# Performance work log

Hardware: AMD Instinct MI355X
Metric: run time of the kernel (lower is better)

## Reference

```python
import jax, jax.numpy as jnp
import numpy as np

B, D, K, H = 8192, 1024, 8, 2048


def setup_inputs() -> dict:
    key = jax.random.key(0)
    ks = jax.random.split(key, 4)
    x = jax.random.normal(ks[0], (B, D), dtype=jnp.float32)
    centroids = jax.random.normal(ks[1], (K, D), dtype=jnp.float32)
    W1 = jax.random.normal(ks[2], (K, D, H), dtype=jnp.float32) / np.sqrt(D).astype(np.float32)
    b1 = jnp.zeros((K, H), dtype=jnp.float32)
    W2 = jax.random.normal(ks[3], (K, H), dtype=jnp.float32) / np.sqrt(H).astype(np.float32)
    b2 = jnp.zeros((K,), dtype=jnp.float32)
    return {"x": x, "centroids": centroids, "W1": W1, "b1": b1, "W2": W2, "b2": b2}


def reference(x, centroids, W1, b1, W2, b2):
    # --- k-means hard routing: nearest centroid per sample (euclidean max_sim) ---
    # d2[b,k] = ||x_b||^2 - 2 x_b . c_k + ||c_k||^2  (avoid [B,K,D] blowup)
    d2 = (jnp.sum(x * x, axis=-1, keepdims=True)
          - 2.0 * (x @ centroids.T)
          + jnp.sum(centroids * centroids, axis=-1)[None, :])  # [B, K]
    cluster = jnp.argmin(d2, axis=-1)  # [B] int, hard assignment

    # --- per-expert log-likelihood heads (Einet stand-in), computed densely ---
    h = jnp.tanh(jnp.einsum("bd,kdh->kbh", x, W1) + b1[:, None, :])  # [K, B, H]
    lls = jnp.einsum("kbh,kh->kb", h, W2) + b2[:, None]              # [K, B]

    # --- combine: each sample takes the LL from its routed expert, original order ---
    lls_sorted = jnp.take_along_axis(lls.T, cluster[:, None], axis=1)[:, 0]  # [B]
    return lls_sorted
```

## Files before the change

### kernel.cpp

```cpp
#include <hip/hip_runtime.h>
#include <hip/hip_bf16.h>
#include <stdint.h>

#define B_N 8192
#define D_N 1024
#define K_N 8
#define H_N 2048

#define BM 352
#define BN 256
#define BK 64
#define GRID_MT 32
#define ABUF 45056
#define BUFSZ 77824
#define RO_OFF 155648
#define PLL_OFF 157056
#define GEMM_LDS 162688

typedef unsigned int u32;
typedef unsigned short u16;
typedef __attribute__((ext_vector_type(8))) short short8;
typedef __attribute__((ext_vector_type(4))) float float4v;

struct __align__(8) us4 { u16 x, y, z, w; };

__device__ __forceinline__ u16 f2bf(float f) {
    union { float f; u32 u; } v; v.f = f;
    u32 u = v.u;
    u32 r = (u + 0x7fffu + ((u >> 16) & 1u)) >> 16;
    return (u16)r;
}

__device__ __forceinline__ float fast_tanh(float x) {
    float t = __expf(2.0f * x);
    return 1.0f - 2.0f * __builtin_amdgcn_rcpf(t + 1.0f);
}

__device__ __forceinline__ void async_copy16(void* lds, const void* g) {
    __builtin_amdgcn_global_load_lds(
        (const __attribute__((address_space(1))) void*)g,
        (__attribute__((address_space(3))) void*)lds, 16, 0, 0);
}

__global__ void route_kernel(const float* __restrict__ x,
                             const float* __restrict__ cent,
                             u16* __restrict__ xbf,
                             int* __restrict__ cluster,
                             u32* __restrict__ counts) {
    int tid = threadIdx.x;
    if (blockIdx.x == 0 && tid < K_N) counts[tid * 32] = 0;
    int wave = tid >> 6, lane = tid & 63;
    int b = blockIdx.x * 4 + wave;
    const float* xr = x + (size_t)b * D_N;

    float4 xv[4];
#pragma unroll
    for (int i = 0; i < 4; ++i)
        xv[i] = *(const float4*)(xr + i * 256 + lane * 4);

#pragma unroll
    for (int i = 0; i < 4; ++i) {
        us4 o;
        o.x = f2bf(xv[i].x); o.y = f2bf(xv[i].y);
        o.z = f2bf(xv[i].z); o.w = f2bf(xv[i].w);
        *(us4*)(xbf + (size_t)b * D_N + i * 256 + lane * 4) = o;
    }

    double acc[K_N];
#pragma unroll
    for (int k = 0; k < K_N; ++k) {
        const float* cr = cent + k * D_N;
        double s = 0.0;
#pragma unroll
        for (int i = 0; i < 4; ++i) {
            float4 cv = *(const float4*)(cr + i * 256 + lane * 4);
            double d0 = (double)xv[i].x - (double)cv.x; s += d0 * d0;
            double d1 = (double)xv[i].y - (double)cv.y; s += d1 * d1;
            double d2 = (double)xv[i].z - (double)cv.z; s += d2 * d2;
            double d3 = (double)xv[i].w - (double)cv.w; s += d3 * d3;
        }
        acc[k] = s;
    }
#pragma unroll
    for (int k = 0; k < K_N; ++k) {
        double v = acc[k];
        for (int off = 32; off; off >>= 1) v += __shfl_down(v, off);
        acc[k] = v;
    }
    if (lane == 0) {
        int best = 0; double bv = acc[0];
#pragma unroll
        for (int k = 1; k < K_N; ++k)
            if (acc[k] < bv) { bv = acc[k]; best = k; }
        cluster[b] = best;
    }
}

__global__ void scatter_kernel(const int* __restrict__ cluster,
                               u32* __restrict__ counts,
                               u32* __restrict__ idxl) {
    __shared__ u32 wcnt[4][K_N];
    __shared__ u32 gb[K_N];
    int tid = threadIdx.x;
    int b = blockIdx.x * 256 + tid;
    int lane = tid & 63, wid = tid >> 6;
    int cl = cluster[b];
    unsigned long long lower = (1ull << lane) - 1ull;
    u32 rank = 0;
#pragma unroll
    for (int k = 0; k < K_N; ++k) {
        unsigned long long mk = __ballot(cl == k);
        if (k == cl) rank = (u32)__popcll(mk & lower);
        if (lane == 0) wcnt[wid][k] = (u32)__popcll(mk);
    }
    __syncthreads();
    if (tid < K_N) {
        u32 tot = wcnt[0][tid] + wcnt[1][tid] + wcnt[2][tid] + wcnt[3][tid];
        gb[tid] = atomicAdd(&counts[tid * 32], tot);
    }
    __syncthreads();
    u32 woff = 0;
    if (wid > 0) woff += wcnt[0][cl];
    if (wid > 1) woff += wcnt[1][cl];
    if (wid > 2) woff += wcnt[2][cl];
    idxl[(size_t)cl * B_N + gb[cl] + woff + rank] = (u32)b;
}

__global__ void w1t_kernel(const float* __restrict__ w1, u16* __restrict__ w1t) {
    __shared__ float ts[64][65];
    int tid = threadIdx.x;
    int h0 = blockIdx.x * 64, d0 = blockIdx.y * 64, k = blockIdx.z;
    const float* src = w1 + ((size_t)k * D_N + d0) * H_N + h0;
#pragma unroll
    for (int i = 0; i < 4; ++i) {
        int q = i * 256 + tid;
        int r = q >> 4, c4 = (q & 15) * 4;
        float4 v = *(const float4*)(src + (size_t)r * H_N + c4);
        ts[c4 + 0][r] = v.x; ts[c4 + 1][r] = v.y;
        ts[c4 + 2][r] = v.z; ts[c4 + 3][r] = v.w;
    }
    __syncthreads();
    u16* dst = w1t + ((size_t)k * H_N + h0) * D_N + d0;
#pragma unroll
    for (int i = 0; i < 4; ++i) {
        int q = i * 256 + tid;
        int hr = q >> 4, d4 = (q & 15) * 4;
        us4 o;
        o.x = f2bf(ts[hr][d4 + 0]); o.y = f2bf(ts[hr][d4 + 1]);
        o.z = f2bf(ts[hr][d4 + 2]); o.w = f2bf(ts[hr][d4 + 3]);
        *(us4*)(dst + (size_t)hr * D_N + d4) = o;
    }
}

__global__ __launch_bounds__(512, 2) void gemm_kernel(
                            const u16* __restrict__ xbf,
                            const u16* __restrict__ w1t,
                            const float* __restrict__ b1,
                            const float* __restrict__ w2,
                            const u32* __restrict__ idxl,
                            const u32* __restrict__ counts,
                            float* __restrict__ llp) {
    extern __shared__ char lds[];
    int k = -1, mt = 0, ntile = 0;
#pragma unroll
    for (int kk = 0; kk < K_N; ++kk) {
        int c = (int)counts[kk * 32];
        int t = (c + BM - 1) / BM;
        if ((int)blockIdx.x >= ntile && (int)blockIdx.x < ntile + t) { k = kk; mt = (int)blockIdx.x - ntile; }
        ntile += t;
    }
    if (k < 0) return;
    int cnt = (int)counts[k * 32];
    int nc = blockIdx.y;
    int rows = cnt - mt * BM; if (rows > BM) rows = BM;
    int tid = threadIdx.x;
    int lane = tid & 63, w = tid >> 6;
    int wm = w >> 2, wn = w & 3;
    int wmbase = wm * 176;
    int h0 = nc * BN;
    int l15 = lane & 15, l4 = lane >> 4;

    u32* ro = (u32*)(lds + RO_OFF);
    float* pll = (float*)(lds + PLL_OFF);

    if (tid < BM) {
        int m = mt * BM + tid;
        int mm = m < cnt ? m : cnt - 1;
        ro[tid] = idxl[(size_t)k * B_N + mm] * (u32)(D_N * 2);
    }
    __syncthreads();

    u32 srcA[6], srcB[4];
#pragma unroll
    for (int i = 0; i < 5; ++i) {
        int c = i * 512 + tid; int r = c >> 3, j = c & 7;
        srcA[i] = ro[r] + ((u32)(j ^ (r & 7)) << 4);
    }
    {
        int c = (tid & 255); int r = 320 + (c >> 3), j = c & 7;
        srcA[5] = ro[r] + ((u32)(j ^ (r & 7)) << 4);
    }
#pragma unroll
    for (int i = 0; i < 4; ++i) {
        int c = i * 512 + tid; int r = c >> 3, j = c & 7;
        srcB[i] = ((u32)(k * H_N + h0 + r) << 11) + ((u32)(j ^ (r & 7)) << 4);
    }
    const char* xb = (const char*)xbf;
    const char* wb = (const char*)w1t;

    float4v acc[11][4];
#pragma unroll
    for (int mf = 0; mf < 11; ++mf)
#pragma unroll
        for (int nf = 0; nf < 4; ++nf)
            acc[mf][nf] = (float4v){0.f, 0.f, 0.f, 0.f};

#pragma unroll
    for (int i = 0; i < 5; ++i)
        async_copy16(lds + i * 8192 + w * 1024, xb + srcA[i]);
    if (w < 4)
        async_copy16(lds + 5 * 8192 + w * 1024, xb + srcA[5]);
#pragma unroll
    for (int i = 0; i < 4; ++i)
        async_copy16(lds + ABUF + i * 8192 + w * 1024, wb + srcB[i]);
    __syncthreads();

    for (int t = 0; t < 16; ++t) {
        char* Acur = lds + (t & 1) * BUFSZ;
        char* Bcur = Acur + ABUF;
        char* Anxt = lds + ((t + 1) & 1) * BUFSZ;
        char* Bnxt = Anxt + ABUF;
        u32 doff = (u32)((t + 1) << 7);
        bool pre = (t < 15);

        if (pre) {
            async_copy16(Anxt + 0 * 8192 + w * 1024, xb + srcA[0] + doff);
            async_copy16(Anxt + 1 * 8192 + w * 1024, xb + srcA[1] + doff);
            async_copy16(Anxt + 2 * 8192 + w * 1024, xb + srcA[2] + doff);
            async_copy16(Anxt + 3 * 8192 + w * 1024, xb + srcA[3] + doff);
            async_copy16(Anxt + 4 * 8192 + w * 1024, xb + srcA[4] + doff);
            if (w < 4)
                async_copy16(Anxt + 5 * 8192 + w * 1024, xb + srcA[5] + doff);
        }

#pragma unroll
        for (int kk = 0; kk < 2; ++kk) {
            short8 bf[4];
#pragma unroll
            for (int nf = 0; nf < 4; ++nf) {
                int rb = wn * 64 + nf * 16 + l15;
                bf[nf] = *(const short8*)(Bcur + rb * 128 + (((kk * 4 + l4) ^ (rb & 7)) << 4));
            }
            if (kk == 1 && pre) {
                async_copy16(Bnxt + 0 * 8192 + w * 1024, wb + srcB[0] + doff);
                async_copy16(Bnxt + 1 * 8192 + w * 1024, wb + srcB[1] + doff);
                async_copy16(Bnxt + 2 * 8192 + w * 1024, wb + srcB[2] + doff);
                async_copy16(Bnxt + 3 * 8192 + w * 1024, wb + srcB[3] + doff);
            }
            __builtin_amdgcn_s_setprio(1);
#pragma unroll
            for (int mf = 0; mf < 11; ++mf) {
                if ((wmbase + mf * 16) < rows) {
                    int r0 = wmbase + mf * 16 + l15;
                    short8 a = *(const short8*)(Acur + r0 * 128 + (((kk * 4 + l4) ^ (r0 & 7)) << 4));
#pragma unroll
                    for (int nf = 0; nf < 4; ++nf)
                        acc[mf][nf] = __builtin_amdgcn_mfma_f32_16x16x32_bf16(a, bf[nf], acc[mf][nf], 0, 0, 0);
                }
            }
            __builtin_amdgcn_s_setprio(0);
        }
        __syncthreads();
    }

    float w2v[4], b1v[4];
#pragma unroll
    for (int nf = 0; nf < 4; ++nf) {
        int h = h0 + wn * 64 + nf * 16 + l15;
        w2v[nf] = w2[k * H_N + h];
        b1v[nf] = b1[k * H_N + h];
    }
#pragma unroll
    for (int mf = 0; mf < 11; ++mf) {
        float rs[4] = {0.f, 0.f, 0.f, 0.f};
#pragma unroll
        for (int nf = 0; nf < 4; ++nf) {
#pragma unroll
            for (int r = 0; r < 4; ++r)
                rs[r] += fast_tanh(acc[mf][nf][r] + b1v[nf]) * w2v[nf];
        }
#pragma unroll
        for (int r = 0; r < 4; ++r) {
            float v = rs[r];
            v += __shfl_xor(v, 8);
            v += __shfl_xor(v, 4);
            v += __shfl_xor(v, 2);
            v += __shfl_xor(v, 1);
            if (l15 == 0) pll[wn * 352 + wmbase + mf * 16 + l4 * 4 + r] = v;
        }
    }
    __syncthreads();
    if (tid < BM) {
        int m = mt * BM + tid;
        if (m < cnt) {
            u32 b = idxl[(size_t)k * B_N + m];
            llp[(size_t)nc * B_N + b] = pll[tid] + pll[352 + tid] + pll[704 + tid] + pll[1056 + tid];
        }
    }
}

__global__ void combine_kernel(const float* __restrict__ llp,
                               const int* __restrict__ cluster,
                               const float* __restrict__ b2,
                               float* __restrict__ out) {
    int b = blockIdx.x * 256 + threadIdx.x;
    float s = b2[cluster[b]];
#pragma unroll
    for (int nc = 0; nc < 8; ++nc) s += llp[(size_t)nc * B_N + b];
    out[b] = s;
}

extern "C" void kernel_launch(void* const* d_in, const int* in_sizes, int n_in,
                              void* d_out, int out_size, void* d_ws, size_t ws_size,
                              hipStream_t stream) {
    const float* x    = (const float*)d_in[0];
    const float* cent = (const float*)d_in[1];
    const float* W1   = (const float*)d_in[2];
    const float* b1   = (const float*)d_in[3];
    const float* W2   = (const float*)d_in[4];
    const float* b2   = (const float*)d_in[5];
    float* out = (float*)d_out;

    char* ws = (char*)d_ws;
    u16* xbf     = (u16*)(ws + 0);
    u16* w1t     = (u16*)(ws + 16777216);
    u32* counts  = (u32*)(ws + 50331648);
    int* cluster = (int*)(ws + 50332672);
    u32* idxl    = (u32*)(ws + 50365440);
    float* llp   = (float*)(ws + 50627584);

    (void)hipFuncSetAttribute((const void*)gemm_kernel,
                              hipFuncAttributeMaxDynamicSharedMemorySize, GEMM_LDS);

    hipLaunchKernelGGL(route_kernel, dim3(B_N / 4), dim3(256), 0, stream,
                       x, cent, xbf, cluster, counts);
    hipLaunchKernelGGL(scatter_kernel, dim3(32), dim3(256), 0, stream,
                       cluster, counts, idxl);
    hipLaunchKernelGGL(w1t_kernel, dim3(H_N / 64, D_N / 64, K_N), dim3(256), 0, stream,
                       W1, w1t);
    hipLaunchKernelGGL(gemm_kernel, dim3(GRID_MT, 8), dim3(512), GEMM_LDS, stream,
                       xbf, w1t, b1, W2, idxl, counts, llp);
    hipLaunchKernelGGL(combine_kernel, dim3(B_N / 256), dim3(256), 0, stream,
                       llp, cluster, b2, out);
}
```

Measured before the change: 87.34 us.

## Switch GEMM to four-stage BK=32 async pipeline with explicit vmcnt waits

Replaces the double-buffered BK=64 main loop with a four-buffer ring of BK=32 tiles, keeping three tiles of loads in flight. __syncthreads is replaced by manual s_waitcnt vmcnt counts plus raw barriers, so each wait covers only the oldest stage. The LDS layout changes so that each 16-row fragment is contiguous, with a new XOR swizzle and a precomputed per-lane fragment offset. The aim is to hide global-load latency more deeply, at the cost of twice as many barriers and hand-tuned wait counts that break if the number of loads per stage changes.

```diff
diff --git a/kernel.cpp b/kernel.cpp
--- a/kernel.cpp
+++ b/kernel.cpp
@@ -9,10 +9,9 @@
 
 #define BM 352
 #define BN 256
-#define BK 64
 #define GRID_MT 32
-#define ABUF 45056
-#define BUFSZ 77824
+#define ABUF 22528
+#define BUFSZ 38912
 #define RO_OFF 155648
 #define PLL_OFF 157056
 #define GEMM_LDS 162688
@@ -190,24 +189,32 @@
     }
     __syncthreads();
 
-    u32 srcA[6], srcB[4];
-#pragma unroll
-    for (int i = 0; i < 5; ++i) {
-        int c = i * 512 + tid; int r = c >> 3, j = c & 7;
-        srcA[i] = ro[r] + ((u32)(j ^ (r & 7)) << 4);
-    }
-    {
-        int c = (tid & 255); int r = 320 + (c >> 3), j = c & 7;
-        srcA[5] = ro[r] + ((u32)(j ^ (r & 7)) << 4);
-    }
-#pragma unroll
-    for (int i = 0; i < 4; ++i) {
-        int c = i * 512 + tid; int r = c >> 3, j = c & 7;
-        srcB[i] = ((u32)(k * H_N + h0 + r) << 11) + ((u32)(j ^ (r & 7)) << 4);
+    u32 srcA[3], srcB[2];
+#pragma unroll
+    for (int i = 0; i < 2; ++i) {
+        int c = (i * 8 + w) * 64 + lane;
+        int row2 = c >> 3, u = (c & 7) ^ (row2 & 7);
+        srcA[i] = ro[row2 * 2 + (u >> 2)] + (u32)((u & 3) << 4);
+    }
+    if (w < 6) {
+        int c = (16 + w) * 64 + lane;
+        int row2 = c >> 3, u = (c & 7) ^ (row2 & 7);
+        srcA[2] = ro[row2 * 2 + (u >> 2)] + (u32)((u & 3) << 4);
+    } else {
+        srcA[2] = 0;
+    }
+#pragma unroll
+    for (int i = 0; i < 2; ++i) {
+        int c = (i * 8 + w) * 64 + lane;
+        int row2 = c >> 3, u = (c & 7) ^ (row2 & 7);
+        srcB[i] = ((u32)(k * H_N + h0 + row2 * 2 + (u >> 2)) << 11) + (u32)((u & 3) << 4);
     }
     const char* xb = (const char*)xbf;
     const char* wb = (const char*)w1t;
 
+    int sw = (((l15 & 1) << 2) | l4) ^ ((l15 >> 1) & 7);
+    u32 foff = (u32)(((l15 >> 1) << 7) | (sw << 4));
+
     float4v acc[11][4];
 #pragma unroll
     for (int mf = 0; mf < 11; ++mf)
@@ -215,63 +222,65 @@
         for (int nf = 0; nf < 4; ++nf)
             acc[mf][nf] = (float4v){0.f, 0.f, 0.f, 0.f};
 
-#pragma unroll
-    for (int i = 0; i < 5; ++i)
-        async_copy16(lds + i * 8192 + w * 1024, xb + srcA[i]);
-    if (w < 4)
-        async_copy16(lds + 5 * 8192 + w * 1024, xb + srcA[5]);
-#pragma unroll
-    for (int i = 0; i < 4; ++i)
-        async_copy16(lds + ABUF + i * 8192 + w * 1024, wb + srcB[i]);
-    __syncthreads();
-
-    for (int t = 0; t < 16; ++t) {
-        char* Acur = lds + (t & 1) * BUFSZ;
-        char* Bcur = Acur + ABUF;
-        char* Anxt = lds + ((t + 1) & 1) * BUFSZ;
-        char* Bnxt = Anxt + ABUF;
-        u32 doff = (u32)((t + 1) << 7);
-        bool pre = (t < 15);
-
-        if (pre) {
-            async_copy16(Anxt + 0 * 8192 + w * 1024, xb + srcA[0] + doff);
-            async_copy16(Anxt + 1 * 8192 + w * 1024, xb + srcA[1] + doff);
-            async_copy16(Anxt + 2 * 8192 + w * 1024, xb + srcA[2] + doff);
-            async_copy16(Anxt + 3 * 8192 + w * 1024, xb + srcA[3] + doff);
-            async_copy16(Anxt + 4 * 8192 + w * 1024, xb + srcA[4] + doff);
-            if (w < 4)
-                async_copy16(Anxt + 5 * 8192 + w * 1024, xb + srcA[5] + doff);
-        }
-
-#pragma unroll
-        for (int kk = 0; kk < 2; ++kk) {
-            short8 bf[4];
-#pragma unroll
-            for (int nf = 0; nf < 4; ++nf) {
-                int rb = wn * 64 + nf * 16 + l15;
-                bf[nf] = *(const short8*)(Bcur + rb * 128 + (((kk * 4 + l4) ^ (rb & 7)) << 4));
+    auto stage_tile = [&](int tt) {
+        char* An = lds + (tt & 3) * BUFSZ;
+        char* Bn = An + ABUF;
+        u32 d = (u32)(tt << 6);
+        async_copy16(An + w * 1024,           xb + srcA[0] + d);
+        async_copy16(An + 8192 + w * 1024,    xb + srcA[1] + d);
+        if (w < 6)
+            async_copy16(An + 16384 + w * 1024, xb + srcA[2] + d);
+        async_copy16(Bn + w * 1024,           wb + srcB[0] + d);
+        async_copy16(Bn + 8192 + w * 1024,    wb + srcB[1] + d);
+    };
+
+    auto compute_tile = [&](int t) {
+        const char* Acur = lds + (t & 3) * BUFSZ;
+        const char* Af = Acur + wmbase * 64 + foff;
+        const char* Bf = Acur + ABUF + (wn << 12) + foff;
+        short8 bfv[4];
+#pragma unroll
+        for (int nf = 0; nf < 4; ++nf)
+            bfv[nf] = *(const short8*)(Bf + nf * 1024);
+        __builtin_amdgcn_s_setprio(1);
+#pragma unroll
+        for (int mf = 0; mf < 11; ++mf) {
+            if ((wmbase + mf * 16) < rows) {
+                short8 a = *(const short8*)(Af + mf * 1024);
+#pragma unroll
+                for (int nf = 0; nf < 4; ++nf)
+                    acc[mf][nf] = __builtin_amdgcn_mfma_f32_16x16x32_bf16(a, bfv[nf], acc[mf][nf], 0, 0, 0);
             }
-            if (kk == 1 && pre) {
-                async_copy16(Bnxt + 0 * 8192 + w * 1024, wb + srcB[0] + doff);
-                async_copy16(Bnxt + 1 * 8192 + w * 1024, wb + srcB[1] + doff);
-                async_copy16(Bnxt + 2 * 8192 + w * 1024, wb + srcB[2] + doff);
-                async_copy16(Bnxt + 3 * 8192 + w * 1024, wb + srcB[3] + doff);
-            }
-            __builtin_amdgcn_s_setprio(1);
-#pragma unroll
-            for (int mf = 0; mf < 11; ++mf) {
-                if ((wmbase + mf * 16) < rows) {
-                    int r0 = wmbase + mf * 16 + l15;
-                    short8 a = *(const short8*)(Acur + r0 * 128 + (((kk * 4 + l4) ^ (r0 & 7)) << 4));
-#pragma unroll
-                    for (int nf = 0; nf < 4; ++nf)
-                        acc[mf][nf] = __builtin_amdgcn_mfma_f32_16x16x32_bf16(a, bf[nf], acc[mf][nf], 0, 0, 0);
-                }
-            }
-            __builtin_amdgcn_s_setprio(0);
-        }
-        __syncthreads();
-    }
+        }
+        __builtin_amdgcn_s_setprio(0);
+    };
+
+#define WAITV(NL, NH) do { \
+        if (w < 6) asm volatile("s_waitcnt vmcnt(" #NL ") lgkmcnt(0)" ::: "memory"); \
+        else       asm volatile("s_waitcnt vmcnt(" #NH ") lgkmcnt(0)" ::: "memory"); \
+    } while (0)
+#define BAR() do { __builtin_amdgcn_s_barrier(); asm volatile("" ::: "memory"); } while (0)
+
+    stage_tile(0); stage_tile(1); stage_tile(2);
+    WAITV(10, 8);
+    BAR();
+
+    for (int t = 0; t < 29; ++t) {
+        stage_tile(t + 3);
+        compute_tile(t);
+        WAITV(10, 8);
+        BAR();
+    }
+    compute_tile(29);
+    WAITV(5, 4);
+    BAR();
+    compute_tile(30);
+    asm volatile("s_waitcnt vmcnt(0) lgkmcnt(0)" ::: "memory");
+    BAR();
+    compute_tile(31);
+
+#undef WAITV
+#undef BAR
 
     float w2v[4], b1v[4];
 #pragma unroll
```

New measurement: 91.94 us. 1.05x slower.

## Restructure GEMM main loop into four barrier-pinned phases with interleaved async loads

Applied to the files above, without the earlier changes.

Shrinks the M tile from 352 to 320 rows (10 MFMA fragments per wave instead of 11) and rewrites the K loop into four explicit phases. Each phase loads its A/B fragments from LDS, issues a slice of the next tile's global-to-LDS async copies, waits on lgkmcnt, then runs 20 MFMAs at raised priority. The aim is a fixed LDS-read/MFMA/copy interleave that spreads global traffic across the iteration, at the cost of more raw barriers and more M tiles in the grid.

```diff
diff --git a/kernel.cpp b/kernel.cpp
--- a/kernel.cpp
+++ b/kernel.cpp
@@ -7,15 +7,15 @@
 #define K_N 8
 #define H_N 2048
 
-#define BM 352
+#define BM 320
 #define BN 256
 #define BK 64
-#define GRID_MT 32
-#define ABUF 45056
-#define BUFSZ 77824
-#define RO_OFF 155648
-#define PLL_OFF 157056
-#define GEMM_LDS 162688
+#define GRID_MT 34
+#define ABYTES 40960
+#define BUFSZ 73728
+#define RO_OFF 147456
+#define PLL_OFF 148736
+#define GEMM_LDS 153856
 
 typedef unsigned int u32;
 typedef unsigned short u16;
@@ -176,7 +176,7 @@
     int tid = threadIdx.x;
     int lane = tid & 63, w = tid >> 6;
     int wm = w >> 2, wn = w & 3;
-    int wmbase = wm * 176;
+    int wmbase = wm * 160;
     int h0 = nc * BN;
     int l15 = lane & 15, l4 = lane >> 4;
 
@@ -190,16 +190,12 @@
     }
     __syncthreads();
 
-    u32 srcA[6], srcB[4];
+    u32 srcA[5], srcB[4];
 #pragma unroll
     for (int i = 0; i < 5; ++i) {
         int c = i * 512 + tid; int r = c >> 3, j = c & 7;
         srcA[i] = ro[r] + ((u32)(j ^ (r & 7)) << 4);
     }
-    {
-        int c = (tid & 255); int r = 320 + (c >> 3), j = c & 7;
-        srcA[5] = ro[r] + ((u32)(j ^ (r & 7)) << 4);
-    }
 #pragma unroll
     for (int i = 0; i < 4; ++i) {
         int c = i * 512 + tid; int r = c >> 3, j = c & 7;
@@ -208,70 +204,101 @@
     const char* xb = (const char*)xbf;
     const char* wb = (const char*)w1t;
 
-    float4v acc[11][4];
-#pragma unroll
-    for (int mf = 0; mf < 11; ++mf)
+    int swz = l15 & 7;
+    u32 aB0 = (u32)((wmbase + l15) * 128 + (((0 + l4) ^ swz) << 4));
+    u32 aB1 = (u32)((wmbase + l15) * 128 + (((4 + l4) ^ swz) << 4));
+    u32 bB0 = (u32)(ABYTES + (wn * 64 + l15) * 128 + (((0 + l4) ^ swz) << 4));
+    u32 bB1 = (u32)(ABYTES + (wn * 64 + l15) * 128 + (((4 + l4) ^ swz) << 4));
+
+    float4v acc[10][4];
+#pragma unroll
+    for (int mf = 0; mf < 10; ++mf)
 #pragma unroll
         for (int nf = 0; nf < 4; ++nf)
             acc[mf][nf] = (float4v){0.f, 0.f, 0.f, 0.f};
 
-#pragma unroll
-    for (int i = 0; i < 5; ++i)
-        async_copy16(lds + i * 8192 + w * 1024, xb + srcA[i]);
-    if (w < 4)
-        async_copy16(lds + 5 * 8192 + w * 1024, xb + srcA[5]);
-#pragma unroll
-    for (int i = 0; i < 4; ++i)
-        async_copy16(lds + ABUF + i * 8192 + w * 1024, wb + srcB[i]);
-    __syncthreads();
+#define STA(BUF, I, D) async_copy16((BUF) + (I) * 8192 + w * 1024, xb + srcA[I] + (D))
+#define STB(BUF, I, D) async_copy16((BUF) + ABYTES + (I) * 8192 + w * 1024, wb + srcB[I] + (D))
+#define BAR() do { asm volatile("" ::: "memory"); __builtin_amdgcn_s_barrier(); \
+                   asm volatile("" ::: "memory"); } while (0)
+#define LGKM0_PIN() do { asm volatile("s_waitcnt lgkmcnt(0)" ::: "memory"); \
+                         __builtin_amdgcn_sched_barrier(0); } while (0)
+#define MFMA_PHASE(MFB, BREG)                                                    \
+    do {                                                                         \
+        __builtin_amdgcn_s_setprio(1);                                           \
+        _Pragma("unroll")                                                        \
+        for (int i_ = 0; i_ < 5; ++i_) {                                         \
+            if (wmbase + ((MFB) + i_) * 16 < rows) {                             \
+                _Pragma("unroll")                                                \
+                for (int nf_ = 0; nf_ < 4; ++nf_)                                \
+                    acc[(MFB) + i_][nf_] = __builtin_amdgcn_mfma_f32_16x16x32_bf16( \
+                        a[i_], BREG[nf_], acc[(MFB) + i_][nf_], 0, 0, 0);        \
+            }                                                                    \
+        }                                                                        \
+        __builtin_amdgcn_s_setprio(0);                                           \
+    } while (0)
+
+    {
+        char* Bp = lds;
+        STA(Bp, 0, 0); STA(Bp, 1, 0); STA(Bp, 2, 0); STA(Bp, 3, 0); STA(Bp, 4, 0);
+        STB(Bp, 0, 0); STB(Bp, 1, 0); STB(Bp, 2, 0); STB(Bp, 3, 0);
+    }
 
     for (int t = 0; t < 16; ++t) {
-        char* Acur = lds + (t & 1) * BUFSZ;
-        char* Bcur = Acur + ABUF;
-        char* Anxt = lds + ((t + 1) & 1) * BUFSZ;
-        char* Bnxt = Anxt + ABUF;
-        u32 doff = (u32)((t + 1) << 7);
+        const char* Acur = lds + (t & 1) * BUFSZ;
+        char* Bnx = lds + ((t + 1) & 1) * BUFSZ;
+        u32 d = (u32)((t + 1) << 7);
         bool pre = (t < 15);
-
-        if (pre) {
-            async_copy16(Anxt + 0 * 8192 + w * 1024, xb + srcA[0] + doff);
-            async_copy16(Anxt + 1 * 8192 + w * 1024, xb + srcA[1] + doff);
-            async_copy16(Anxt + 2 * 8192 + w * 1024, xb + srcA[2] + doff);
-            async_copy16(Anxt + 3 * 8192 + w * 1024, xb + srcA[3] + doff);
-            async_copy16(Anxt + 4 * 8192 + w * 1024, xb + srcA[4] + doff);
-            if (w < 4)
-                async_copy16(Anxt + 5 * 8192 + w * 1024, xb + srcA[5] + doff);
-        }
-
-#pragma unroll
-        for (int kk = 0; kk < 2; ++kk) {
-            short8 bf[4];
-#pragma unroll
-            for (int nf = 0; nf < 4; ++nf) {
-                int rb = wn * 64 + nf * 16 + l15;
-                bf[nf] = *(const short8*)(Bcur + rb * 128 + (((kk * 4 + l4) ^ (rb & 7)) << 4));
-            }
-            if (kk == 1 && pre) {
-                async_copy16(Bnxt + 0 * 8192 + w * 1024, wb + srcB[0] + doff);
-                async_copy16(Bnxt + 1 * 8192 + w * 1024, wb + srcB[1] + doff);
-                async_copy16(Bnxt + 2 * 8192 + w * 1024, wb + srcB[2] + doff);
-                async_copy16(Bnxt + 3 * 8192 + w * 1024, wb + srcB[3] + doff);
-            }
-            __builtin_amdgcn_s_setprio(1);
-#pragma unroll
-            for (int mf = 0; mf < 11; ++mf) {
-                if ((wmbase + mf * 16) < rows) {
-                    int r0 = wmbase + mf * 16 + l15;
-                    short8 a = *(const short8*)(Acur + r0 * 128 + (((kk * 4 + l4) ^ (r0 & 7)) << 4));
-#pragma unroll
-                    for (int nf = 0; nf < 4; ++nf)
-                        acc[mf][nf] = __builtin_amdgcn_mfma_f32_16x16x32_bf16(a, bf[nf], acc[mf][nf], 0, 0, 0);
-                }
-            }
-            __builtin_amdgcn_s_setprio(0);
-        }
-        __syncthreads();
-    }
+        short8 a[5], bC[4];
+
+        asm volatile("s_waitcnt vmcnt(0)" ::: "memory");
+        BAR();
+#pragma unroll
+        for (int nf = 0; nf < 4; ++nf)
+            bC[nf] = *(const short8*)(Acur + bB0 + nf * 2048);
+#pragma unroll
+        for (int i = 0; i < 5; ++i)
+            a[i] = *(const short8*)(Acur + aB0 + i * 2048);
+        if (pre) { STB(Bnx, 0, d); STB(Bnx, 1, d); STB(Bnx, 2, d); }
+        BAR();
+        LGKM0_PIN();
+        MFMA_PHASE(0, bC);
+
+        BAR();
+#pragma unroll
+        for (int i = 0; i < 5; ++i)
+            a[i] = *(const short8*)(Acur + aB0 + (5 + i) * 2048);
+        if (pre) { STB(Bnx, 3, d); STA(Bnx, 0, d); STA(Bnx, 1, d); }
+        BAR();
+        LGKM0_PIN();
+        MFMA_PHASE(5, bC);
+
+        BAR();
+#pragma unroll
+        for (int nf = 0; nf < 4; ++nf)
+            bC[nf] = *(const short8*)(Acur + bB1 + nf * 2048);
+#pragma unroll
+        for (int i = 0; i < 5; ++i)
+            a[i] = *(const short8*)(Acur + aB1 + i * 2048);
+        if (pre) { STA(Bnx, 2, d); STA(Bnx, 3, d); STA(Bnx, 4, d); }
+        BAR();
+        LGKM0_PIN();
+        MFMA_PHASE(0, bC);
+
+        BAR();
+#pragma unroll
+        for (int i = 0; i < 5; ++i)
+            a[i] = *(const short8*)(Acur + aB1 + (5 + i) * 2048);
+        BAR();
+        LGKM0_PIN();
+        MFMA_PHASE(5, bC);
+    }
+
+#undef STA
+#undef STB
+#undef BAR
+#undef LGKM0_PIN
+#undef MFMA_PHASE
 
     float w2v[4], b1v[4];
 #pragma unroll
@@ -281,7 +308,7 @@
         b1v[nf] = b1[k * H_N + h];
     }
 #pragma unroll
-    for (int mf = 0; mf < 11; ++mf) {
+    for (int mf = 0; mf < 10; ++mf) {
         float rs[4] = {0.f, 0.f, 0.f, 0.f};
 #pragma unroll
         for (int nf = 0; nf < 4; ++nf) {
@@ -296,7 +323,7 @@
             v += __shfl_xor(v, 4);
             v += __shfl_xor(v, 2);
             v += __shfl_xor(v, 1);
-            if (l15 == 0) pll[wn * 352 + wmbase + mf * 16 + l4 * 4 + r] = v;
+            if (l15 == 0) pll[wn * 320 + wmbase + mf * 16 + l4 * 4 + r] = v;
         }
     }
     __syncthreads();
@@ -304,7 +331,7 @@
         int m = mt * BM + tid;
         if (m < cnt) {
             u32 b = idxl[(size_t)k * B_N + m];
-            llp[(size_t)nc * B_N + b] = pll[tid] + pll[352 + tid] + pll[704 + tid] + pll[1056 + tid];
+            llp[(size_t)nc * B_N + b] = pll[tid] + pll[320 + tid] + pll[640 + tid] + pll[960 + tid];
         }
     }
 }
```

New measurement: 87.06 us. No clear change (-0.3%).
